# Kernel tuning notes

Hardware: AMD Instinct MI355X
Metric: run time of the kernel (lower is better)

Reference implementation:

```python
import jax, jax.numpy as jnp
import numpy as np

N_NODES = 100000
N_EDGES = 1200000
EMBED_DIM = 64
N_LAYERS = 3


def setup_inputs() -> dict:
    key = jax.random.key(0)
    k1, k2, k3, k4 = jax.random.split(key, 4)
    embeddings = jax.random.normal(k1, (N_NODES, EMBED_DIM), dtype=jnp.float32)
    edge_weight = jax.random.uniform(k2, (N_EDGES,), dtype=jnp.float32)
    edge_src = jax.random.randint(k3, (N_EDGES,), 0, N_NODES, dtype=jnp.int32)
    edge_dst = jax.random.randint(k4, (N_EDGES,), 0, N_NODES, dtype=jnp.int32)
    return {"embeddings": embeddings, "edge_weight": edge_weight,
            "edge_src": edge_src, "edge_dst": edge_dst}


def _spmm(edge_src, edge_dst, edge_weight, x):
    # (A @ x)[d] = sum_{e: dst(e)=d} w[e] * x[src(e)]  -- COO SpMM via gather + segment_sum
    msgs = edge_weight[:, None] * x[edge_src]  # [E, D]
    return jax.ops.segment_sum(msgs, edge_dst, num_segments=N_NODES)


def reference(embeddings, edge_weight, edge_src, edge_dst):
    all_embeddings = [embeddings]
    ego = embeddings
    for _ in range(N_LAYERS):
        ego = _spmm(edge_src, edge_dst, edge_weight, ego)
        all_embeddings.append(ego)
    # stack layer outputs: [n_layers+1, N, D]
    return jnp.stack(all_embeddings, axis=0)
```

## Files before the change

kernel.cpp:

```cpp
#include <hip/hip_runtime.h>


#define N_NODES 100000
#define DIM 64
#define SCAN_CHUNK 1024

#define NR 8
#define RSIZE ((N_NODES + NR - 1) / NR)
#define SLICES 128

typedef int   vint4   __attribute__((ext_vector_type(4)));
typedef float vfloat4 __attribute__((ext_vector_type(4)));


__global__ void hist_range_kernel(const int* __restrict__ edst, int* __restrict__ deg,
                                  int E, int chunk) {
    const int r = blockIdx.x & (NR - 1);
    const int s = blockIdx.x / NR;
    const int lo = r * RSIZE;
    const int hi = min(lo + RSIZE, N_NODES);
    const int e0 = s * chunk;
    if (e0 >= E) return;
    const int e1 = min(e0 + chunk, E);
    const int nv = (e1 - e0) >> 2;
    const vint4* d4 = (const vint4*)(edst + e0);
    for (int i = threadIdx.x; i < nv; i += blockDim.x) {
        vint4 d = __builtin_nontemporal_load(d4 + i);
        #pragma unroll
        for (int j = 0; j < 4; ++j) {
            int dj = d[j];
            if (dj >= lo && dj < hi) atomicAdd(&deg[dj], 1);
        }
    }
    for (int e = e0 + (nv << 2) + threadIdx.x; e < e1; e += blockDim.x) {
        int dj = edst[e];
        if (dj >= lo && dj < hi) atomicAdd(&deg[dj], 1);
    }
}

__global__ void scan1_kernel(const int* __restrict__ deg, int* __restrict__ off,
                             int* __restrict__ bsum, int n) {
    __shared__ int sdata[256];
    int tid = threadIdx.x;
    int base = blockIdx.x * SCAN_CHUNK + tid * 4;
    int v[4];
    #pragma unroll
    for (int i = 0; i < 4; ++i) v[i] = (base + i < n) ? deg[base + i] : 0;
    int tsum = v[0] + v[1] + v[2] + v[3];
    sdata[tid] = tsum;
    __syncthreads();
    for (int d = 1; d < 256; d <<= 1) {
        int t = (tid >= d) ? sdata[tid - d] : 0;
        __syncthreads();
        sdata[tid] += t;
        __syncthreads();
    }
    int excl = sdata[tid] - tsum;
    if (tid == 255) bsum[blockIdx.x] = sdata[255];
    int run = excl;
    #pragma unroll
    for (int i = 0; i < 4; ++i) {
        if (base + i < n) off[base + i] = run;
        run += v[i];
    }
}

__global__ void scan2_kernel(int* __restrict__ bsum, int nb) {
    __shared__ int s[128];
    int tid = threadIdx.x;
    int v = (tid < nb) ? bsum[tid] : 0;
    s[tid] = v;
    __syncthreads();
    for (int d = 1; d < 128; d <<= 1) {
        int t = (tid >= d) ? s[tid - d] : 0;
        __syncthreads();
        s[tid] += t;
        __syncthreads();
    }
    if (tid < nb) bsum[tid] = s[tid] - v;
}

__global__ void scan3_kernel(int* __restrict__ off, const int* __restrict__ bsum, int n) {
    int i = blockIdx.x * blockDim.x + threadIdx.x;
    if (i < n) off[i] += bsum[i / SCAN_CHUNK];
}

__global__ void scatter_range_kernel(const int* __restrict__ esrc, const int* __restrict__ edst,
                                     const float* __restrict__ ew, const int* __restrict__ off,
                                     int* __restrict__ cur, int2* __restrict__ pairs,
                                     int E, int chunk) {
    const int r = blockIdx.x & (NR - 1);
    const int s = blockIdx.x / NR;
    const int lo = r * RSIZE;
    const int hi = min(lo + RSIZE, N_NODES);
    const int e0 = s * chunk;
    if (e0 >= E) return;
    const int e1 = min(e0 + chunk, E);
    const int nv = (e1 - e0) >> 2;
    const vint4*   s4 = (const vint4*)(esrc + e0);
    const vint4*   d4 = (const vint4*)(edst + e0);
    const vfloat4* w4 = (const vfloat4*)(ew + e0);
    for (int i = threadIdx.x; i < nv; i += blockDim.x) {
        vint4 dd = __builtin_nontemporal_load(d4 + i);
        vint4 ss = __builtin_nontemporal_load(s4 + i);
        vfloat4 ww = __builtin_nontemporal_load(w4 + i);
        #pragma unroll
        for (int j = 0; j < 4; ++j) {
            int dj = dd[j];
            if (dj >= lo && dj < hi) {
                int p = off[dj] + atomicAdd(&cur[dj], 1);
                int2 pr;
                pr.x = ss[j];
                pr.y = __float_as_int(ww[j]);
                pairs[p] = pr;
            }
        }
    }
    for (int e = e0 + (nv << 2) + threadIdx.x; e < e1; e += blockDim.x) {
        int dj = edst[e];
        if (dj >= lo && dj < hi) {
            int p = off[dj] + atomicAdd(&cur[dj], 1);
            int2 pr;
            pr.x = esrc[e];
            pr.y = __float_as_int(ew[e]);
            pairs[p] = pr;
        }
    }
}


__global__ void spmm_csr_kernel(const float* __restrict__ x,
                                const int2* __restrict__ pairs,
                                const int* __restrict__ off,
                                const int* __restrict__ deg,
                                float* __restrict__ y) {
    int gtid = blockIdx.x * blockDim.x + threadIdx.x;
    int node = gtid >> 6;
    int lane = threadIdx.x & 63;
    int o  = lane >> 3;
    int ol = lane & 7;
    if (node >= N_NODES) return;
    int s0 = off[node];
    int n  = deg[node];
    float4 a0 = make_float4(0.f, 0.f, 0.f, 0.f);
    float4 a1 = make_float4(0.f, 0.f, 0.f, 0.f);
    for (int k = o; k < n; k += 8) {
        int2 pr = pairs[s0 + k];
        float w = __int_as_float(pr.y);
        const float4* row = (const float4*)(x + (size_t)pr.x * DIM);
        float4 v0 = row[ol];
        float4 v1 = row[ol + 8];
        a0.x += w * v0.x; a0.y += w * v0.y; a0.z += w * v0.z; a0.w += w * v0.w;
        a1.x += w * v1.x; a1.y += w * v1.y; a1.z += w * v1.z; a1.w += w * v1.w;
    }
    #pragma unroll
    for (int d = 8; d <= 32; d <<= 1) {
        a0.x += __shfl_xor(a0.x, d); a0.y += __shfl_xor(a0.y, d);
        a0.z += __shfl_xor(a0.z, d); a0.w += __shfl_xor(a0.w, d);
        a1.x += __shfl_xor(a1.x, d); a1.y += __shfl_xor(a1.y, d);
        a1.z += __shfl_xor(a1.z, d); a1.w += __shfl_xor(a1.w, d);
    }
    if (o == 0) {
        vfloat4* yrow = (vfloat4*)(y + (size_t)node * DIM);
        vfloat4 r0 = { a0.x, a0.y, a0.z, a0.w };
        vfloat4 r1 = { a1.x, a1.y, a1.z, a1.w };
        __builtin_nontemporal_store(r0, yrow + ol);
        __builtin_nontemporal_store(r1, yrow + ol + 8);
    }
}


__global__ void spmm_atomic_kernel(const float* __restrict__ x, const float* __restrict__ ew,
                                   const int* __restrict__ esrc, const int* __restrict__ edst,
                                   float* __restrict__ y, int n_edges) {
    long long tid = (long long)blockIdx.x * blockDim.x + threadIdx.x;
    int e = (int)(tid >> 6);
    int d = (int)(tid & 63);
    if (e >= n_edges) return;
    int s = esrc[e]; int t = edst[e]; float w = ew[e];
    atomicAdd(&y[(long long)t * DIM + d], w * x[(long long)s * DIM + d]);
}

extern "C" void kernel_launch(void* const* d_in, const int* in_sizes, int n_in,
                              void* d_out, int out_size, void* d_ws, size_t ws_size,
                              hipStream_t stream) {
    const float* emb  = (const float*)d_in[0];
    const float* ew   = (const float*)d_in[1];
    const int*   esrc = (const int*)d_in[2];
    const int*   edst = (const int*)d_in[3];
    float* out = (float*)d_out;

    const int E = in_sizes[1];
    const size_t layer_elems = (size_t)N_NODES * DIM;

    size_t need = (size_t)E * 8 + (size_t)3 * N_NODES * 4 + 512;
    hipMemcpyAsync(out, emb, layer_elems * sizeof(float), hipMemcpyDeviceToDevice, stream);

    if (ws_size >= need) {
        char* w = (char*)d_ws;
        int2* pairs = (int2*)w;
        int* deg  = (int*)(w + (size_t)E * 8);
        int* cur  = deg + N_NODES;
        int* off  = cur + N_NODES;
        int* bsum = off + N_NODES;

        hipMemsetAsync(deg, 0, (size_t)2 * N_NODES * 4, stream);

        const int chunk = (((E + SLICES - 1) / SLICES) + 3) & ~3;
        const int rblocks = NR * SLICES;

        hist_range_kernel<<<rblocks, 256, 0, stream>>>(edst, deg, E, chunk);

        const int nscan = (N_NODES + SCAN_CHUNK - 1) / SCAN_CHUNK;
        scan1_kernel<<<nscan, 256, 0, stream>>>(deg, off, bsum, N_NODES);
        scan2_kernel<<<1, 128, 0, stream>>>(bsum, nscan);
        scan3_kernel<<<(N_NODES + 255) / 256, 256, 0, stream>>>(off, bsum, N_NODES);

        scatter_range_kernel<<<rblocks, 256, 0, stream>>>(esrc, edst, ew, off, cur, pairs, E, chunk);

        const int nb = (N_NODES + 3) / 4;
        for (int l = 1; l <= 3; ++l) {
            spmm_csr_kernel<<<nb, 256, 0, stream>>>(
                out + (size_t)(l - 1) * layer_elems, pairs, off, deg,
                out + (size_t)l * layer_elems);
        }
    } else {
        hipMemsetAsync(out + layer_elems, 0, 3 * layer_elems * sizeof(float), stream);
        const long long total_threads = (long long)E * 64;
        const int blocks = (int)((total_threads + 255) / 256);
        for (int l = 1; l <= 3; ++l) {
            spmm_atomic_kernel<<<blocks, 256, 0, stream>>>(
                out + (size_t)(l - 1) * layer_elems, ew, esrc, edst,
                out + (size_t)l * layer_elems, E);
        }
    }
}
```

Before: 392.7 us.

## Bind scatter node ranges to XCD id with ticket-based slice claiming

The range-partitioned histogram becomes a plain one-pass atomic histogram over all destinations. The scatter kernel now reads the hardware XCC id so that each chiplet handles one destination range, keeping the cursor atomics inside that XCD's L2. Blocks claim edge slices dynamically through per-XCD tickets. The cursor array is seeded with the offsets in scan3, which removes one memset and the offset load in the scatter. This relies on the XCC id register and on blocks being spread evenly across the XCDs. If any XCD hosts no blocks, its node range is never scattered.

```diff
diff --git a/kernel.cpp b/kernel.cpp
--- a/kernel.cpp
+++ b/kernel.cpp
@@ -7,34 +7,30 @@
 
 #define NR 8
 #define RSIZE ((N_NODES + NR - 1) / NR)
-#define SLICES 128
+#define SLICES 256
 
 typedef int   vint4   __attribute__((ext_vector_type(4)));
 typedef float vfloat4 __attribute__((ext_vector_type(4)));
 
-
-__global__ void hist_range_kernel(const int* __restrict__ edst, int* __restrict__ deg,
-                                  int E, int chunk) {
-    const int r = blockIdx.x & (NR - 1);
-    const int s = blockIdx.x / NR;
-    const int lo = r * RSIZE;
-    const int hi = min(lo + RSIZE, N_NODES);
-    const int e0 = s * chunk;
-    if (e0 >= E) return;
-    const int e1 = min(e0 + chunk, E);
-    const int nv = (e1 - e0) >> 2;
-    const vint4* d4 = (const vint4*)(edst + e0);
-    for (int i = threadIdx.x; i < nv; i += blockDim.x) {
-        vint4 d = __builtin_nontemporal_load(d4 + i);
-        #pragma unroll
-        for (int j = 0; j < 4; ++j) {
-            int dj = d[j];
-            if (dj >= lo && dj < hi) atomicAdd(&deg[dj], 1);
-        }
-    }
-    for (int e = e0 + (nv << 2) + threadIdx.x; e < e1; e += blockDim.x) {
-        int dj = edst[e];
-        if (dj >= lo && dj < hi) atomicAdd(&deg[dj], 1);
+__device__ __forceinline__ int xcd_id() {
+    int x;
+    asm volatile("s_getreg_b32 %0, hwreg(HW_REG_XCC_ID)" : "=s"(x));
+    return x & (NR - 1);
+}
+
+
+__global__ void hist_kernel(const int* __restrict__ edst, int* __restrict__ deg, int E) {
+    int i = blockIdx.x * blockDim.x + threadIdx.x;
+    int nv = E >> 2;
+    if (i < nv) {
+        vint4 d = __builtin_nontemporal_load(((const vint4*)edst) + i);
+        atomicAdd(&deg[d[0]], 1);
+        atomicAdd(&deg[d[1]], 1);
+        atomicAdd(&deg[d[2]], 1);
+        atomicAdd(&deg[d[3]], 1);
+    }
+    if (i == 0) {
+        for (int e = nv << 2; e < E; ++e) atomicAdd(&deg[edst[e]], 1);
     }
 }
 
@@ -80,50 +76,62 @@
     if (tid < nb) bsum[tid] = s[tid] - v;
 }
 
-__global__ void scan3_kernel(int* __restrict__ off, const int* __restrict__ bsum, int n) {
+__global__ void scan3_kernel(int* __restrict__ off, int* __restrict__ cur,
+                             const int* __restrict__ bsum, int n) {
     int i = blockIdx.x * blockDim.x + threadIdx.x;
-    if (i < n) off[i] += bsum[i / SCAN_CHUNK];
-}
-
-__global__ void scatter_range_kernel(const int* __restrict__ esrc, const int* __restrict__ edst,
-                                     const float* __restrict__ ew, const int* __restrict__ off,
-                                     int* __restrict__ cur, int2* __restrict__ pairs,
-                                     int E, int chunk) {
-    const int r = blockIdx.x & (NR - 1);
-    const int s = blockIdx.x / NR;
+    if (i < n) {
+        int v = off[i] + bsum[i / SCAN_CHUNK];
+        off[i] = v;
+        cur[i] = v;
+    }
+}
+
+__global__ void scatter_xcd_kernel(const int* __restrict__ esrc, const int* __restrict__ edst,
+                                   const float* __restrict__ ew, int* __restrict__ cur,
+                                   int2* __restrict__ pairs, int* __restrict__ ticket,
+                                   int E, int chunk) {
+    const int r = xcd_id();
     const int lo = r * RSIZE;
     const int hi = min(lo + RSIZE, N_NODES);
-    const int e0 = s * chunk;
-    if (e0 >= E) return;
-    const int e1 = min(e0 + chunk, E);
-    const int nv = (e1 - e0) >> 2;
-    const vint4*   s4 = (const vint4*)(esrc + e0);
-    const vint4*   d4 = (const vint4*)(edst + e0);
-    const vfloat4* w4 = (const vfloat4*)(ew + e0);
-    for (int i = threadIdx.x; i < nv; i += blockDim.x) {
-        vint4 dd = __builtin_nontemporal_load(d4 + i);
-        vint4 ss = __builtin_nontemporal_load(s4 + i);
-        vfloat4 ww = __builtin_nontemporal_load(w4 + i);
-        #pragma unroll
-        for (int j = 0; j < 4; ++j) {
-            int dj = dd[j];
+    __shared__ int s_sl;
+    for (;;) {
+        if (threadIdx.x == 0) s_sl = atomicAdd(&ticket[r], 1);
+        __syncthreads();
+        const int s = s_sl;
+        __syncthreads();
+        if (s >= SLICES) return;
+        const int e0 = s * chunk;
+        if (e0 >= E) continue;
+        const int e1 = min(e0 + chunk, E);
+        const int nv = (e1 - e0) >> 2;
+        const vint4*   s4 = (const vint4*)(esrc + e0);
+        const vint4*   d4 = (const vint4*)(edst + e0);
+        const vfloat4* w4 = (const vfloat4*)(ew + e0);
+        for (int i = threadIdx.x; i < nv; i += blockDim.x) {
+            vint4 dd = __builtin_nontemporal_load(d4 + i);
+            vint4 ss = __builtin_nontemporal_load(s4 + i);
+            vfloat4 ww = __builtin_nontemporal_load(w4 + i);
+            #pragma unroll
+            for (int j = 0; j < 4; ++j) {
+                int dj = dd[j];
+                if (dj >= lo && dj < hi) {
+                    int p = atomicAdd(&cur[dj], 1);
+                    int2 pr;
+                    pr.x = ss[j];
+                    pr.y = __float_as_int(ww[j]);
+                    pairs[p] = pr;
+                }
+            }
+        }
+        for (int e = e0 + (nv << 2) + threadIdx.x; e < e1; e += blockDim.x) {
+            int dj = edst[e];
             if (dj >= lo && dj < hi) {
-                int p = off[dj] + atomicAdd(&cur[dj], 1);
+                int p = atomicAdd(&cur[dj], 1);
                 int2 pr;
-                pr.x = ss[j];
-                pr.y = __float_as_int(ww[j]);
+                pr.x = esrc[e];
+                pr.y = __float_as_int(ew[e]);
                 pairs[p] = pr;
             }
-        }
-    }
-    for (int e = e0 + (nv << 2) + threadIdx.x; e < e1; e += blockDim.x) {
-        int dj = edst[e];
-        if (dj >= lo && dj < hi) {
-            int p = off[dj] + atomicAdd(&cur[dj], 1);
-            int2 pr;
-            pr.x = esrc[e];
-            pr.y = __float_as_int(ew[e]);
-            pairs[p] = pr;
         }
     }
 }
@@ -193,30 +201,31 @@
     const int E = in_sizes[1];
     const size_t layer_elems = (size_t)N_NODES * DIM;
 
-    size_t need = (size_t)E * 8 + (size_t)3 * N_NODES * 4 + 512;
+    size_t need = (size_t)E * 8 + (size_t)3 * N_NODES * 4 + 1024;
     hipMemcpyAsync(out, emb, layer_elems * sizeof(float), hipMemcpyDeviceToDevice, stream);
 
     if (ws_size >= need) {
         char* w = (char*)d_ws;
         int2* pairs = (int2*)w;
-        int* deg  = (int*)(w + (size_t)E * 8);
-        int* cur  = deg + N_NODES;
-        int* off  = cur + N_NODES;
-        int* bsum = off + N_NODES;
-
-        hipMemsetAsync(deg, 0, (size_t)2 * N_NODES * 4, stream);
-
-        const int chunk = (((E + SLICES - 1) / SLICES) + 3) & ~3;
-        const int rblocks = NR * SLICES;
-
-        hist_range_kernel<<<rblocks, 256, 0, stream>>>(edst, deg, E, chunk);
+        int* deg    = (int*)(w + (size_t)E * 8);
+        int* cur    = deg + N_NODES;
+        int* off    = cur + N_NODES;
+        int* bsum   = off + N_NODES;
+        int* ticket = bsum + 128;
+
+        hipMemsetAsync(deg, 0, (size_t)N_NODES * 4, stream);
+        hipMemsetAsync(ticket, 0, NR * 4, stream);
+
+        const int nv4 = E >> 2;
+        hist_kernel<<<(nv4 + 255) / 256, 256, 0, stream>>>(edst, deg, E);
 
         const int nscan = (N_NODES + SCAN_CHUNK - 1) / SCAN_CHUNK;
         scan1_kernel<<<nscan, 256, 0, stream>>>(deg, off, bsum, N_NODES);
         scan2_kernel<<<1, 128, 0, stream>>>(bsum, nscan);
-        scan3_kernel<<<(N_NODES + 255) / 256, 256, 0, stream>>>(off, bsum, N_NODES);
-
-        scatter_range_kernel<<<rblocks, 256, 0, stream>>>(esrc, edst, ew, off, cur, pairs, E, chunk);
+        scan3_kernel<<<(N_NODES + 255) / 256, 256, 0, stream>>>(off, cur, bsum, N_NODES);
+
+        const int chunk = (((E + SLICES - 1) / SLICES) + 3) & ~3;
+        scatter_xcd_kernel<<<1024, 256, 0, stream>>>(esrc, edst, ew, cur, pairs, ticket, E, chunk);
 
         const int nb = (N_NODES + 3) / 4;
         for (int l = 1; l <= 3; ++l) {
```

Result: slower. 405.6 us (+3.3%).
